# Performance work log

Measured on AMD Instinct MI355X. Metric: run time of the kernel, lower is better.

## Reference

```python
import jax, jax.numpy as jnp
import numpy as np

B, N = 8, 50000
NB, NA, NT, NI, NC = 60000, 120000, 180000, 20000, 1500000


def _term_index(key, n_terms, arity, n_atoms):
    # distinct atom indices per term (avoids degenerate zero-length vectors)
    k1, k2 = jax.random.split(key)
    base = jax.random.randint(k1, (n_terms,), 0, n_atoms)
    cols = [base]
    for a in range(arity - 1):
        off = jax.random.randint(jax.random.fold_in(k2, a), (n_terms,), 1, n_atoms)
        cols.append((base + off + a) % n_atoms)
    return jnp.stack(cols, axis=1).astype(jnp.int32)


def setup_inputs() -> dict:
    key = jax.random.key(0)
    ks = jax.random.split(key, 24)
    u = lambda k, s, lo, hi: jax.random.uniform(k, s, jnp.float32, lo, hi)
    coords = jax.random.normal(ks[0], (B, N, 3), jnp.float32) * 10.0
    return dict(
        coords=coords,
        bond_index=_term_index(ks[1], NB, 2, N),
        bond_rest_length=u(ks[2], (NB,), 1.0, 2.0),
        bond_force_constant=u(ks[3], (NB,), 200.0, 800.0),
        angle_index=_term_index(ks[4], NA, 3, N),
        angle_force_constant=u(ks[5], (NA,), 50.0, 300.0),
        angle_c0=u(ks[6], (NA,), 0.5, 2.0),
        angle_c1=u(ks[7], (NA,), -1.0, 1.0),
        angle_c2=u(ks[8], (NA,), -1.0, 1.0),
        torsion_index=_term_index(ks[9], NT, 4, N),
        torsion_force_constant=u(ks[10], (NT,), 1.0, 20.0),
        torsion_order=jax.random.randint(ks[11], (NT,), 1, 7).astype(jnp.int32),
        torsion_cos_term=jnp.where(jax.random.bernoulli(ks[12], 0.5, (NT,)), 1.0, -1.0).astype(jnp.float32),
        inversion_index=_term_index(ks[13], NI, 4, N),
        inversion_force_constant=u(ks[14], (NI,), 1.0, 40.0),
        inversion_c0=u(ks[15], (NI,), 0.5, 1.5),
        inversion_c1=u(ks[16], (NI,), -1.0, 1.0),
        inversion_c2=u(ks[17], (NI,), -1.0, 1.0),
        nonbond_index=_term_index(ks[18], NC, 2, N),
        vdw_minimum=u(ks[19], (NC,), 3.0, 4.0),
        vdw_well_depth=u(ks[20], (NC,), 0.01, 0.2),
        vdw_threshold_sq=jnp.square(u(ks[21], (NC,), 10.0, 30.0)),
    )


def _uff_energy(coords, bond_index, bond_rest_length, bond_force_constant,
                angle_index, angle_force_constant, angle_c0, angle_c1, angle_c2,
                torsion_index, torsion_force_constant, torsion_order, torsion_cos_term,
                inversion_index, inversion_force_constant, inversion_c0, inversion_c1, inversion_c2,
                nonbond_index, vdw_minimum, vdw_well_depth, vdw_threshold_sq):
    take = lambda idx: jnp.take(coords, idx, axis=1)  # (B, P, 3)

    # ---- bond stretch: 0.5 * k * (|r_ij| - r0)^2 ----
    d = take(bond_index[:, 0]) - take(bond_index[:, 1])
    dist = jnp.sqrt(jnp.sum(d * d, -1))
    e_bond = jnp.sum(0.5 * bond_force_constant * jnp.square(dist - bond_rest_length), -1)

    # ---- angle bend (general cosine expansion, order == 0 branch) ----
    p1, p2, p3 = take(angle_index[:, 0]), take(angle_index[:, 1]), take(angle_index[:, 2])
    v1, v2 = p1 - p2, p3 - p2
    dot = jnp.sum(v1 * v2, -1)
    inv = jax.lax.rsqrt(jnp.maximum(jnp.sum(v1 * v1, -1) * jnp.sum(v2 * v2, -1), 1e-24))
    ct = jnp.clip(dot * inv, -0.999999, 0.999999)
    cs = ct * ct
    ss = jnp.maximum(1.0 - cs, 1e-12)
    e_angle = jnp.sum(angle_force_constant * (angle_c0 + angle_c1 * ct + angle_c2 * (cs - ss)), -1)

    # ---- torsion: 0.5 * V * (1 - cos_term * cos(n * phi)) ----
    q1, q2, q3, q4 = (take(torsion_index[:, a]) for a in range(4))
    b1, b2, b3 = q2 - q1, q3 - q2, q4 - q3
    n1 = jnp.cross(b1, b2)
    n2 = jnp.cross(b2, b3)
    cn = jnp.sum(n1 * n2, -1) * jax.lax.rsqrt(
        jnp.maximum(jnp.sum(n1 * n1, -1) * jnp.sum(n2 * n2, -1), 1e-24))
    phi = jnp.arccos(jnp.clip(cn, -0.999999, 0.999999))
    n_f = torsion_order.astype(coords.dtype)
    e_tor = jnp.sum(0.5 * torsion_force_constant * (1.0 - torsion_cos_term * jnp.cos(n_f * phi)), -1)

    # ---- inversion (Wilson angle): K*(c0 + c1*sinY + c2*(2*sinY^2 - 1)), central atom = col 1 ----
    cA = take(inversion_index[:, 1])
    rji = take(inversion_index[:, 0]) - cA
    rjk = take(inversion_index[:, 2]) - cA
    rjl = take(inversion_index[:, 3]) - cA
    nrm = jnp.cross(rji, rjk)
    cosY = jnp.sum(nrm * rjl, -1) * jax.lax.rsqrt(
        jnp.maximum(jnp.sum(nrm * nrm, -1) * jnp.sum(rjl * rjl, -1), 1e-24))
    cosY = jnp.clip(cosY, -0.999999, 0.999999)
    sinY = jnp.sqrt(jnp.maximum(1.0 - cosY * cosY, 0.0))
    e_inv = jnp.sum(inversion_force_constant * (inversion_c0 + inversion_c1 * sinY
                                                + inversion_c2 * (2.0 * sinY * sinY - 1.0)), -1)

    # ---- vdW LJ on radius-graph candidates: D*((R/r)^12 - 2*(R/r)^6) within cutoff ----
    dnb = take(nonbond_index[:, 0]) - take(nonbond_index[:, 1])
    d2 = jnp.sum(dnb * dnb, -1)
    within = d2 <= vdw_threshold_sq  # pair selection done under no_grad in the original
    x2 = jnp.square(vdw_minimum) / jnp.maximum(d2, 1e-12)
    x6 = x2 * x2 * x2
    e_pair = vdw_well_depth * (x6 * x6 - 2.0 * x6)
    e_vdw = jnp.sum(jnp.where(within, e_pair, 0.0), -1)

    return e_bond + e_angle + e_tor + e_inv + e_vdw  # (B,)


def reference(coords, bond_index, bond_rest_length, bond_force_constant,
              angle_index, angle_force_constant, angle_c0, angle_c1, angle_c2,
              torsion_index, torsion_force_constant, torsion_order, torsion_cos_term,
              inversion_index, inversion_force_constant, inversion_c0, inversion_c1, inversion_c2,
              nonbond_index, vdw_minimum, vdw_well_depth, vdw_threshold_sq):
    return _uff_energy(coords, bond_index, bond_rest_length, bond_force_constant,
                       angle_index, angle_force_constant, angle_c0, angle_c1, angle_c2,
                       torsion_index, torsion_force_constant, torsion_order, torsion_cos_term,
                       inversion_index, inversion_force_constant, inversion_c0, inversion_c1, inversion_c2,
                       nonbond_index, vdw_minimum, vdw_well_depth, vdw_threshold_sq)
```

## Files before the change

kernel.cpp:

```cpp
#include <hip/hip_runtime.h>

#define TPB 256
#define NWAVE (TPB / 64)
#define CHUNK 256
#define GRID_MAIN 2048

typedef int vi2 __attribute__((ext_vector_type(2)));
typedef int vi4 __attribute__((ext_vector_type(4)));

struct SegInfo {
    int cb, ca, ct, ci, cl;
    int NB, NA, NT, NI, NC;
    int N;
};

__device__ __forceinline__ float clamp1(float x) {
    return fminf(fmaxf(x, -0.999999f), 0.999999f);
}

__device__ __forceinline__ float ntf(const float* p) { return __builtin_nontemporal_load(p); }

template <bool USE_WS>
__device__ __forceinline__ float4 loadC(const float4* __restrict__ cw,
                                        const float* __restrict__ coords,
                                        int N, int atom, int b) {
    if (USE_WS) {
        return cw[((size_t)atom << 3) + b];
    } else {
        const float* sp = coords + ((size_t)b * N + atom) * 3;
        return make_float4(sp[0], sp[1], sp[2], 0.f);
    }
}

__global__ void __launch_bounds__(TPB) transpose_coords(const float* __restrict__ coords,
                                                        float4* __restrict__ cw,
                                                        float* __restrict__ out, int N) {
    const int a = blockIdx.x * TPB + threadIdx.x;
    if (blockIdx.x == 0 && threadIdx.x < 8) out[threadIdx.x] = 0.f;
    if (a >= N) return;
#pragma unroll
    for (int b = 0; b < 8; b++) {
        const float* sp = coords + ((size_t)b * N + a) * 3;
        cw[((size_t)a << 3) + b] = make_float4(ntf(sp), ntf(sp + 1), ntf(sp + 2), 0.f);
    }
}

template <bool USE_WS>
__global__ void __launch_bounds__(TPB) uff_kernel(
    const float* __restrict__ coords, const float4* __restrict__ cw,
    const int* __restrict__ bidx, const float* __restrict__ br0, const float* __restrict__ bk,
    const int* __restrict__ aidx, const float* __restrict__ ak,
    const float* __restrict__ ac0, const float* __restrict__ ac1, const float* __restrict__ ac2,
    const int* __restrict__ tidx, const float* __restrict__ tk,
    const int* __restrict__ tord, const float* __restrict__ tcos,
    const int* __restrict__ iidx, const float* __restrict__ ik,
    const float* __restrict__ ic0, const float* __restrict__ ic1, const float* __restrict__ ic2,
    const int* __restrict__ nidx, const float* __restrict__ vmin,
    const float* __restrict__ vdep, const float* __restrict__ vthr,
    float* __restrict__ out, SegInfo s)
{
    __shared__ int4   sI[CHUNK];
    __shared__ float4 sP[CHUNK];

    const int tid = threadIdx.x;
    const int lane = tid & 63;
    const int b = tid & 7;
    const int g = tid >> 3;
    const int N = s.N;
    float acc = 0.f;

    for (int c = blockIdx.x; c < s.cb; c += gridDim.x) {
        const int base = c * CHUNK;
        {
            const int u = min(base + tid, s.NB - 1);
            const vi2 ij = __builtin_nontemporal_load((const vi2*)bidx + u);
            sI[tid] = make_int4(ij.x, ij.y, 0, 0);
            sP[tid] = make_float4(ntf(br0 + u), ntf(bk + u), 0.f, 0.f);
        }
        __syncthreads();
#pragma unroll 2
        for (int j = 0; j < 8; j++) {
            const int slot = g + 32 * j;
            const int4 q = sI[slot];
            const float4 p = sP[slot];
            float4 ci = loadC<USE_WS>(cw, coords, N, q.x, b);
            float4 cj = loadC<USE_WS>(cw, coords, N, q.y, b);
            float dx = ci.x - cj.x, dy = ci.y - cj.y, dz = ci.z - cj.z;
            float dd = sqrtf(dx * dx + dy * dy + dz * dz) - p.x;
            if (base + slot < s.NB) acc += 0.5f * p.y * dd * dd;
        }
        __syncthreads();
    }

    for (int c = blockIdx.x; c < s.ca; c += gridDim.x) {
        const int base = c * CHUNK;
        {
            const int u = min(base + tid, s.NA - 1);
            sI[tid] = make_int4(aidx[3 * u], aidx[3 * u + 1], aidx[3 * u + 2], 0);
            sP[tid] = make_float4(ntf(ak + u), ntf(ac0 + u), ntf(ac1 + u), ntf(ac2 + u));
        }
        __syncthreads();
#pragma unroll 2
        for (int j = 0; j < 8; j++) {
            const int slot = g + 32 * j;
            const int4 q = sI[slot];
            const float4 p = sP[slot];
            float4 P = loadC<USE_WS>(cw, coords, N, q.x, b);
            float4 Q = loadC<USE_WS>(cw, coords, N, q.y, b);
            float4 R = loadC<USE_WS>(cw, coords, N, q.z, b);
            float ax = P.x - Q.x, ay = P.y - Q.y, az = P.z - Q.z;
            float bx = R.x - Q.x, by = R.y - Q.y, bz = R.z - Q.z;
            float dot = ax * bx + ay * by + az * bz;
            float nn = (ax * ax + ay * ay + az * az) * (bx * bx + by * by + bz * bz);
            float ct = clamp1(dot * rsqrtf(fmaxf(nn, 1e-24f)));
            float cs = ct * ct;
            float sb = fmaxf(1.f - cs, 1e-12f);
            if (base + slot < s.NA) acc += p.x * (p.y + p.z * ct + p.w * (cs - sb));
        }
        __syncthreads();
    }

    for (int c = blockIdx.x; c < s.ct; c += gridDim.x) {
        const int base = c * CHUNK;
        {
            const int u = min(base + tid, s.NT - 1);
            const vi4 q = __builtin_nontemporal_load((const vi4*)tidx + u);
            sI[tid] = make_int4(q.x, q.y, q.z, q.w);
            sP[tid] = make_float4(ntf(tk + u), ntf(tcos + u),
                                  __int_as_float(__builtin_nontemporal_load(tord + u)), 0.f);
        }
        __syncthreads();
#pragma unroll 2
        for (int j = 0; j < 8; j++) {
            const int slot = g + 32 * j;
            const int4 q = sI[slot];
            const float4 p = sP[slot];
            const int ord = __float_as_int(p.z);
            float4 P1 = loadC<USE_WS>(cw, coords, N, q.x, b);
            float4 P2 = loadC<USE_WS>(cw, coords, N, q.y, b);
            float4 P3 = loadC<USE_WS>(cw, coords, N, q.z, b);
            float4 P4 = loadC<USE_WS>(cw, coords, N, q.w, b);
            float b1x = P2.x - P1.x, b1y = P2.y - P1.y, b1z = P2.z - P1.z;
            float b2x = P3.x - P2.x, b2y = P3.y - P2.y, b2z = P3.z - P2.z;
            float b3x = P4.x - P3.x, b3y = P4.y - P3.y, b3z = P4.z - P3.z;
            float n1x = b1y * b2z - b1z * b2y;
            float n1y = b1z * b2x - b1x * b2z;
            float n1z = b1x * b2y - b1y * b2x;
            float n2x = b2y * b3z - b2z * b3y;
            float n2y = b2z * b3x - b2x * b3z;
            float n2z = b2x * b3y - b2y * b3x;
            float dot = n1x * n2x + n1y * n2y + n1z * n2z;
            float nn = (n1x * n1x + n1y * n1y + n1z * n1z) *
                       (n2x * n2x + n2y * n2y + n2z * n2z);
            float x = clamp1(dot * rsqrtf(fmaxf(nn, 1e-24f)));
            float Tp = 1.f, Tc = x, res = x;
#pragma unroll
            for (int kk = 2; kk <= 6; kk++) {
                float Tn = 2.f * x * Tc - Tp;
                Tp = Tc; Tc = Tn;
                if (ord == kk) res = Tn;
            }
            if (base + slot < s.NT) acc += 0.5f * p.x * (1.f - p.y * res);
        }
        __syncthreads();
    }

    for (int c = blockIdx.x; c < s.ci; c += gridDim.x) {
        const int base = c * CHUNK;
        {
            const int u = min(base + tid, s.NI - 1);
            const vi4 q = __builtin_nontemporal_load((const vi4*)iidx + u);
            sI[tid] = make_int4(q.x, q.y, q.z, q.w);
            sP[tid] = make_float4(ntf(ik + u), ntf(ic0 + u), ntf(ic1 + u), ntf(ic2 + u));
        }
        __syncthreads();
#pragma unroll 2
        for (int j = 0; j < 8; j++) {
            const int slot = g + 32 * j;
            const int4 q = sI[slot];
            const float4 p = sP[slot];
            float4 CA = loadC<USE_WS>(cw, coords, N, q.y, b);
            float4 PI = loadC<USE_WS>(cw, coords, N, q.x, b);
            float4 PK = loadC<USE_WS>(cw, coords, N, q.z, b);
            float4 PL = loadC<USE_WS>(cw, coords, N, q.w, b);
            float jix = PI.x - CA.x, jiy = PI.y - CA.y, jiz = PI.z - CA.z;
            float jkx = PK.x - CA.x, jky = PK.y - CA.y, jkz = PK.z - CA.z;
            float lx  = PL.x - CA.x, ly  = PL.y - CA.y, lz  = PL.z - CA.z;
            float nx = jiy * jkz - jiz * jky;
            float ny = jiz * jkx - jix * jkz;
            float nz = jix * jky - jiy * jkx;
            float dot = nx * lx + ny * ly + nz * lz;
            float nn = (nx * nx + ny * ny + nz * nz) * (lx * lx + ly * ly + lz * lz);
            float cosY = clamp1(dot * rsqrtf(fmaxf(nn, 1e-24f)));
            float sinY = sqrtf(fmaxf(1.f - cosY * cosY, 0.f));
            if (base + slot < s.NI) acc += p.x * (p.y + p.z * sinY + p.w * (2.f * sinY * sinY - 1.f));
        }
        __syncthreads();
    }

    for (int c = blockIdx.x; c < s.cl; c += gridDim.x) {
        const int base = c * CHUNK;
        {
            const int u = min(base + tid, s.NC - 1);
            const vi2 ij = __builtin_nontemporal_load((const vi2*)nidx + u);
            const float R = ntf(vmin + u);
            sI[tid] = make_int4(ij.x, ij.y, 0, 0);
            sP[tid] = make_float4(R * R, ntf(vdep + u), ntf(vthr + u), 0.f);
        }
        __syncthreads();
#pragma unroll
        for (int j = 0; j < 8; j += 2) {
            const int s0 = g + 32 * j, s1 = s0 + 32;
            const int4 q0 = sI[s0]; const float4 p0 = sP[s0];
            const int4 q1 = sI[s1]; const float4 p1 = sP[s1];
            float4 a0 = loadC<USE_WS>(cw, coords, N, q0.x, b);
            float4 b0 = loadC<USE_WS>(cw, coords, N, q0.y, b);
            float4 a1 = loadC<USE_WS>(cw, coords, N, q1.x, b);
            float4 b1 = loadC<USE_WS>(cw, coords, N, q1.y, b);
            {
                float dx = a0.x - b0.x, dy = a0.y - b0.y, dz = a0.z - b0.z;
                float d2 = dx * dx + dy * dy + dz * dz;
                float x2 = p0.x / fmaxf(d2, 1e-12f);
                float x6 = x2 * x2 * x2;
                float e = p0.y * (x6 * x6 - 2.f * x6);
                if (base + s0 < s.NC && d2 <= p0.z) acc += e;
            }
            {
                float dx = a1.x - b1.x, dy = a1.y - b1.y, dz = a1.z - b1.z;
                float d2 = dx * dx + dy * dy + dz * dz;
                float x2 = p1.x / fmaxf(d2, 1e-12f);
                float x6 = x2 * x2 * x2;
                float e = p1.y * (x6 * x6 - 2.f * x6);
                if (base + s1 < s.NC && d2 <= p1.z) acc += e;
            }
        }
        __syncthreads();
    }

    float v = acc;
    v += __shfl_down(v, 8, 64);
    v += __shfl_down(v, 16, 64);
    v += __shfl_down(v, 32, 64);

    __shared__ float red[NWAVE][8];
    const int wid = tid >> 6;
    if (lane < 8) red[wid][lane] = v;
    __syncthreads();
    if (tid < 8) {
        float ssum = 0.f;
#pragma unroll
        for (int w = 0; w < NWAVE; w++) ssum += red[w][tid];
        atomicAdd(&out[tid], ssum);
    }
}

static inline int cdiv(int a, int b) { return (a + b - 1) / b; }

extern "C" void kernel_launch(void* const* d_in, const int* in_sizes, int n_in,
                              void* d_out, int out_size, void* d_ws, size_t ws_size,
                              hipStream_t stream) {
    const int B = out_size;
    const int NB = in_sizes[2], NA = in_sizes[5], NT = in_sizes[10],
              NI = in_sizes[14], NC = in_sizes[19];
    const int N = in_sizes[0] / (3 * B);

    const float* coords = (const float*)d_in[0];
    const int*   bidx = (const int*)d_in[1];
    const float* br0  = (const float*)d_in[2];
    const float* bk   = (const float*)d_in[3];
    const int*   aidx = (const int*)d_in[4];
    const float* ak   = (const float*)d_in[5];
    const float* ac0  = (const float*)d_in[6];
    const float* ac1  = (const float*)d_in[7];
    const float* ac2  = (const float*)d_in[8];
    const int*   tidx = (const int*)d_in[9];
    const float* tk   = (const float*)d_in[10];
    const int*   tord = (const int*)d_in[11];
    const float* tcos = (const float*)d_in[12];
    const int*   iidx = (const int*)d_in[13];
    const float* ik   = (const float*)d_in[14];
    const float* ic0  = (const float*)d_in[15];
    const float* ic1  = (const float*)d_in[16];
    const float* ic2  = (const float*)d_in[17];
    const int*   nidx = (const int*)d_in[18];
    const float* vmin = (const float*)d_in[19];
    const float* vdep = (const float*)d_in[20];
    const float* vthr = (const float*)d_in[21];

    const size_t ws_need = (size_t)N * 8 * sizeof(float4);
    const bool use_ws = ws_size >= ws_need;
    float4* cw = (float4*)d_ws;

    if (use_ws) {
        transpose_coords<<<cdiv(N, TPB), TPB, 0, stream>>>(coords, cw, (float*)d_out, N);
    } else {
        hipMemsetAsync(d_out, 0, (size_t)out_size * sizeof(float), stream);
    }

    SegInfo s;
    s.NB = NB; s.NA = NA; s.NT = NT; s.NI = NI; s.NC = NC; s.N = N;
    s.cb = cdiv(NB, CHUNK);
    s.ca = cdiv(NA, CHUNK);
    s.ct = cdiv(NT, CHUNK);
    s.ci = cdiv(NI, CHUNK);
    s.cl = cdiv(NC, CHUNK);

    if (use_ws) {
        uff_kernel<true><<<GRID_MAIN, TPB, 0, stream>>>(
            coords, cw, bidx, br0, bk, aidx, ak, ac0, ac1, ac2,
            tidx, tk, tord, tcos, iidx, ik, ic0, ic1, ic2,
            nidx, vmin, vdep, vthr, (float*)d_out, s);
    } else {
        uff_kernel<false><<<GRID_MAIN, TPB, 0, stream>>>(
            coords, cw, bidx, br0, bk, aidx, ak, ac0, ac1, ac2,
            tidx, tk, tord, tcos, iidx, ik, ic0, ic1, ic2,
            nidx, vmin, vdep, vthr, (float*)d_out, s);
    }
}
```

Before: 168.8 us.

## Replace block-strided chunk loops with per-wave dynamic work stealing via atomic counter

Each wavefront now grabs 64-term chunks from a global atomic counter across a unified index space covering all five term types. This replaces the static block-strided loops and their block-wide __syncthreads with per-wave shared staging. The aim is to remove load imbalance between blocks and the barrier stalls between segments. The cost is one atomic per 64 terms, which is about 37k atomics on a single counter, plus branching over the term kind per chunk.

```diff
diff --git a/kernel.cpp b/kernel.cpp
--- a/kernel.cpp
+++ b/kernel.cpp
@@ -2,7 +2,6 @@
 
 #define TPB 256
 #define NWAVE (TPB / 64)
-#define CHUNK 256
 #define GRID_MAIN 2048
 
 typedef int vi2 __attribute__((ext_vector_type(2)));
@@ -19,6 +18,7 @@
 }
 
 __device__ __forceinline__ float ntf(const float* p) { return __builtin_nontemporal_load(p); }
+__device__ __forceinline__ int   nti(const int* p)   { return __builtin_nontemporal_load(p); }
 
 template <bool USE_WS>
 __device__ __forceinline__ float4 loadC(const float4* __restrict__ cw,
@@ -34,9 +34,13 @@
 
 __global__ void __launch_bounds__(TPB) transpose_coords(const float* __restrict__ coords,
                                                         float4* __restrict__ cw,
-                                                        float* __restrict__ out, int N) {
+                                                        float* __restrict__ out,
+                                                        int* __restrict__ ctr, int N) {
     const int a = blockIdx.x * TPB + threadIdx.x;
-    if (blockIdx.x == 0 && threadIdx.x < 8) out[threadIdx.x] = 0.f;
+    if (blockIdx.x == 0) {
+        if (threadIdx.x < 8) out[threadIdx.x] = 0.f;
+        if (threadIdx.x == 8) *ctr = 0;
+    }
     if (a >= N) return;
 #pragma unroll
     for (int b = 0; b < 8; b++) {
@@ -57,184 +61,173 @@
     const float* __restrict__ ic0, const float* __restrict__ ic1, const float* __restrict__ ic2,
     const int* __restrict__ nidx, const float* __restrict__ vmin,
     const float* __restrict__ vdep, const float* __restrict__ vthr,
-    float* __restrict__ out, SegInfo s)
+    int* __restrict__ ctr, float* __restrict__ out, SegInfo s)
 {
-    __shared__ int4   sI[CHUNK];
-    __shared__ float4 sP[CHUNK];
+    __shared__ int4   sI[NWAVE][64];
+    __shared__ float4 sP[NWAVE][64];
 
     const int tid = threadIdx.x;
     const int lane = tid & 63;
-    const int b = tid & 7;
-    const int g = tid >> 3;
+    const int w = tid >> 6;
+    const int b = lane & 7;
+    const int gw = lane >> 3;
     const int N = s.N;
     float acc = 0.f;
 
-    for (int c = blockIdx.x; c < s.cb; c += gridDim.x) {
-        const int base = c * CHUNK;
-        {
-            const int u = min(base + tid, s.NB - 1);
+    int4*   mI = sI[w];
+    float4* mP = sP[w];
+
+    while (true) {
+        int c = 0;
+        if (lane == 0) c = atomicAdd(ctr, 1);
+        c = __shfl(c, 0, 64);
+        if (c >= s.cl) break;
+
+        int kind, base;
+        if (c < s.cb)      { kind = 0; base = c * 64; }
+        else if (c < s.ca) { kind = 1; base = (c - s.cb) * 64; }
+        else if (c < s.ct) { kind = 2; base = (c - s.ca) * 64; }
+        else if (c < s.ci) { kind = 3; base = (c - s.ct) * 64; }
+        else               { kind = 4; base = (c - s.ci) * 64; }
+
+        if (kind == 0) {
+            const int u = min(base + lane, s.NB - 1);
             const vi2 ij = __builtin_nontemporal_load((const vi2*)bidx + u);
-            sI[tid] = make_int4(ij.x, ij.y, 0, 0);
-            sP[tid] = make_float4(ntf(br0 + u), ntf(bk + u), 0.f, 0.f);
-        }
-        __syncthreads();
-#pragma unroll 2
-        for (int j = 0; j < 8; j++) {
-            const int slot = g + 32 * j;
-            const int4 q = sI[slot];
-            const float4 p = sP[slot];
-            float4 ci = loadC<USE_WS>(cw, coords, N, q.x, b);
-            float4 cj = loadC<USE_WS>(cw, coords, N, q.y, b);
-            float dx = ci.x - cj.x, dy = ci.y - cj.y, dz = ci.z - cj.z;
-            float dd = sqrtf(dx * dx + dy * dy + dz * dz) - p.x;
-            if (base + slot < s.NB) acc += 0.5f * p.y * dd * dd;
-        }
-        __syncthreads();
-    }
-
-    for (int c = blockIdx.x; c < s.ca; c += gridDim.x) {
-        const int base = c * CHUNK;
-        {
-            const int u = min(base + tid, s.NA - 1);
-            sI[tid] = make_int4(aidx[3 * u], aidx[3 * u + 1], aidx[3 * u + 2], 0);
-            sP[tid] = make_float4(ntf(ak + u), ntf(ac0 + u), ntf(ac1 + u), ntf(ac2 + u));
-        }
-        __syncthreads();
-#pragma unroll 2
-        for (int j = 0; j < 8; j++) {
-            const int slot = g + 32 * j;
-            const int4 q = sI[slot];
-            const float4 p = sP[slot];
-            float4 P = loadC<USE_WS>(cw, coords, N, q.x, b);
-            float4 Q = loadC<USE_WS>(cw, coords, N, q.y, b);
-            float4 R = loadC<USE_WS>(cw, coords, N, q.z, b);
-            float ax = P.x - Q.x, ay = P.y - Q.y, az = P.z - Q.z;
-            float bx = R.x - Q.x, by = R.y - Q.y, bz = R.z - Q.z;
-            float dot = ax * bx + ay * by + az * bz;
-            float nn = (ax * ax + ay * ay + az * az) * (bx * bx + by * by + bz * bz);
-            float ct = clamp1(dot * rsqrtf(fmaxf(nn, 1e-24f)));
-            float cs = ct * ct;
-            float sb = fmaxf(1.f - cs, 1e-12f);
-            if (base + slot < s.NA) acc += p.x * (p.y + p.z * ct + p.w * (cs - sb));
-        }
-        __syncthreads();
-    }
-
-    for (int c = blockIdx.x; c < s.ct; c += gridDim.x) {
-        const int base = c * CHUNK;
-        {
-            const int u = min(base + tid, s.NT - 1);
+            mI[lane] = make_int4(ij.x, ij.y, 0, 0);
+            mP[lane] = make_float4(ntf(br0 + u), ntf(bk + u), 0.f, 0.f);
+        } else if (kind == 1) {
+            const int u = min(base + lane, s.NA - 1);
+            mI[lane] = make_int4(aidx[3 * u], aidx[3 * u + 1], aidx[3 * u + 2], 0);
+            mP[lane] = make_float4(ntf(ak + u), ntf(ac0 + u), ntf(ac1 + u), ntf(ac2 + u));
+        } else if (kind == 2) {
+            const int u = min(base + lane, s.NT - 1);
             const vi4 q = __builtin_nontemporal_load((const vi4*)tidx + u);
-            sI[tid] = make_int4(q.x, q.y, q.z, q.w);
-            sP[tid] = make_float4(ntf(tk + u), ntf(tcos + u),
-                                  __int_as_float(__builtin_nontemporal_load(tord + u)), 0.f);
-        }
-        __syncthreads();
-#pragma unroll 2
-        for (int j = 0; j < 8; j++) {
-            const int slot = g + 32 * j;
-            const int4 q = sI[slot];
-            const float4 p = sP[slot];
-            const int ord = __float_as_int(p.z);
-            float4 P1 = loadC<USE_WS>(cw, coords, N, q.x, b);
-            float4 P2 = loadC<USE_WS>(cw, coords, N, q.y, b);
-            float4 P3 = loadC<USE_WS>(cw, coords, N, q.z, b);
-            float4 P4 = loadC<USE_WS>(cw, coords, N, q.w, b);
-            float b1x = P2.x - P1.x, b1y = P2.y - P1.y, b1z = P2.z - P1.z;
-            float b2x = P3.x - P2.x, b2y = P3.y - P2.y, b2z = P3.z - P2.z;
-            float b3x = P4.x - P3.x, b3y = P4.y - P3.y, b3z = P4.z - P3.z;
-            float n1x = b1y * b2z - b1z * b2y;
-            float n1y = b1z * b2x - b1x * b2z;
-            float n1z = b1x * b2y - b1y * b2x;
-            float n2x = b2y * b3z - b2z * b3y;
-            float n2y = b2z * b3x - b2x * b3z;
-            float n2z = b2x * b3y - b2y * b3x;
-            float dot = n1x * n2x + n1y * n2y + n1z * n2z;
-            float nn = (n1x * n1x + n1y * n1y + n1z * n1z) *
-                       (n2x * n2x + n2y * n2y + n2z * n2z);
-            float x = clamp1(dot * rsqrtf(fmaxf(nn, 1e-24f)));
-            float Tp = 1.f, Tc = x, res = x;
-#pragma unroll
-            for (int kk = 2; kk <= 6; kk++) {
-                float Tn = 2.f * x * Tc - Tp;
-                Tp = Tc; Tc = Tn;
-                if (ord == kk) res = Tn;
-            }
-            if (base + slot < s.NT) acc += 0.5f * p.x * (1.f - p.y * res);
-        }
-        __syncthreads();
-    }
-
-    for (int c = blockIdx.x; c < s.ci; c += gridDim.x) {
-        const int base = c * CHUNK;
-        {
-            const int u = min(base + tid, s.NI - 1);
+            mI[lane] = make_int4(q.x, q.y, q.z, q.w);
+            mP[lane] = make_float4(ntf(tk + u), ntf(tcos + u),
+                                   __int_as_float(nti(tord + u)), 0.f);
+        } else if (kind == 3) {
+            const int u = min(base + lane, s.NI - 1);
             const vi4 q = __builtin_nontemporal_load((const vi4*)iidx + u);
-            sI[tid] = make_int4(q.x, q.y, q.z, q.w);
-            sP[tid] = make_float4(ntf(ik + u), ntf(ic0 + u), ntf(ic1 + u), ntf(ic2 + u));
-        }
-        __syncthreads();
-#pragma unroll 2
-        for (int j = 0; j < 8; j++) {
-            const int slot = g + 32 * j;
-            const int4 q = sI[slot];
-            const float4 p = sP[slot];
-            float4 CA = loadC<USE_WS>(cw, coords, N, q.y, b);
-            float4 PI = loadC<USE_WS>(cw, coords, N, q.x, b);
-            float4 PK = loadC<USE_WS>(cw, coords, N, q.z, b);
-            float4 PL = loadC<USE_WS>(cw, coords, N, q.w, b);
-            float jix = PI.x - CA.x, jiy = PI.y - CA.y, jiz = PI.z - CA.z;
-            float jkx = PK.x - CA.x, jky = PK.y - CA.y, jkz = PK.z - CA.z;
-            float lx  = PL.x - CA.x, ly  = PL.y - CA.y, lz  = PL.z - CA.z;
-            float nx = jiy * jkz - jiz * jky;
-            float ny = jiz * jkx - jix * jkz;
-            float nz = jix * jky - jiy * jkx;
-            float dot = nx * lx + ny * ly + nz * lz;
-            float nn = (nx * nx + ny * ny + nz * nz) * (lx * lx + ly * ly + lz * lz);
-            float cosY = clamp1(dot * rsqrtf(fmaxf(nn, 1e-24f)));
-            float sinY = sqrtf(fmaxf(1.f - cosY * cosY, 0.f));
-            if (base + slot < s.NI) acc += p.x * (p.y + p.z * sinY + p.w * (2.f * sinY * sinY - 1.f));
-        }
-        __syncthreads();
-    }
-
-    for (int c = blockIdx.x; c < s.cl; c += gridDim.x) {
-        const int base = c * CHUNK;
-        {
-            const int u = min(base + tid, s.NC - 1);
+            mI[lane] = make_int4(q.x, q.y, q.z, q.w);
+            mP[lane] = make_float4(ntf(ik + u), ntf(ic0 + u), ntf(ic1 + u), ntf(ic2 + u));
+        } else {
+            const int u = min(base + lane, s.NC - 1);
             const vi2 ij = __builtin_nontemporal_load((const vi2*)nidx + u);
             const float R = ntf(vmin + u);
-            sI[tid] = make_int4(ij.x, ij.y, 0, 0);
-            sP[tid] = make_float4(R * R, ntf(vdep + u), ntf(vthr + u), 0.f);
+            mI[lane] = make_int4(ij.x, ij.y, 0, 0);
+            mP[lane] = make_float4(R * R, ntf(vdep + u), ntf(vthr + u), 0.f);
         }
-        __syncthreads();
+
+        if (kind == 4) {
 #pragma unroll
-        for (int j = 0; j < 8; j += 2) {
-            const int s0 = g + 32 * j, s1 = s0 + 32;
-            const int4 q0 = sI[s0]; const float4 p0 = sP[s0];
-            const int4 q1 = sI[s1]; const float4 p1 = sP[s1];
-            float4 a0 = loadC<USE_WS>(cw, coords, N, q0.x, b);
-            float4 b0 = loadC<USE_WS>(cw, coords, N, q0.y, b);
-            float4 a1 = loadC<USE_WS>(cw, coords, N, q1.x, b);
-            float4 b1 = loadC<USE_WS>(cw, coords, N, q1.y, b);
-            {
-                float dx = a0.x - b0.x, dy = a0.y - b0.y, dz = a0.z - b0.z;
-                float d2 = dx * dx + dy * dy + dz * dz;
-                float x2 = p0.x / fmaxf(d2, 1e-12f);
-                float x6 = x2 * x2 * x2;
-                float e = p0.y * (x6 * x6 - 2.f * x6);
-                if (base + s0 < s.NC && d2 <= p0.z) acc += e;
-            }
-            {
-                float dx = a1.x - b1.x, dy = a1.y - b1.y, dz = a1.z - b1.z;
-                float d2 = dx * dx + dy * dy + dz * dz;
-                float x2 = p1.x / fmaxf(d2, 1e-12f);
-                float x6 = x2 * x2 * x2;
-                float e = p1.y * (x6 * x6 - 2.f * x6);
-                if (base + s1 < s.NC && d2 <= p1.z) acc += e;
+            for (int j = 0; j < 4; j++) {
+                const int s0 = j * 8 + gw, s1 = s0 + 32;
+                const int4 q0 = mI[s0]; const float4 p0 = mP[s0];
+                const int4 q1 = mI[s1]; const float4 p1 = mP[s1];
+                float4 a0 = loadC<USE_WS>(cw, coords, N, q0.x, b);
+                float4 b0 = loadC<USE_WS>(cw, coords, N, q0.y, b);
+                float4 a1 = loadC<USE_WS>(cw, coords, N, q1.x, b);
+                float4 b1 = loadC<USE_WS>(cw, coords, N, q1.y, b);
+                {
+                    float dx = a0.x - b0.x, dy = a0.y - b0.y, dz = a0.z - b0.z;
+                    float d2 = dx * dx + dy * dy + dz * dz;
+                    float x2 = p0.x / fmaxf(d2, 1e-12f);
+                    float x6 = x2 * x2 * x2;
+                    float e = p0.y * (x6 * x6 - 2.f * x6);
+                    if (base + s0 < s.NC && d2 <= p0.z) acc += e;
+                }
+                {
+                    float dx = a1.x - b1.x, dy = a1.y - b1.y, dz = a1.z - b1.z;
+                    float d2 = dx * dx + dy * dy + dz * dz;
+                    float x2 = p1.x / fmaxf(d2, 1e-12f);
+                    float x6 = x2 * x2 * x2;
+                    float e = p1.y * (x6 * x6 - 2.f * x6);
+                    if (base + s1 < s.NC && d2 <= p1.z) acc += e;
+                }
+            }
+        } else if (kind == 0) {
+#pragma unroll 2
+            for (int j = 0; j < 8; j++) {
+                const int slot = j * 8 + gw;
+                const int4 q = mI[slot]; const float4 p = mP[slot];
+                float4 ci = loadC<USE_WS>(cw, coords, N, q.x, b);
+                float4 cj = loadC<USE_WS>(cw, coords, N, q.y, b);
+                float dx = ci.x - cj.x, dy = ci.y - cj.y, dz = ci.z - cj.z;
+                float dd = sqrtf(dx * dx + dy * dy + dz * dz) - p.x;
+                if (base + slot < s.NB) acc += 0.5f * p.y * dd * dd;
+            }
+        } else if (kind == 1) {
+#pragma unroll 2
+            for (int j = 0; j < 8; j++) {
+                const int slot = j * 8 + gw;
+                const int4 q = mI[slot]; const float4 p = mP[slot];
+                float4 P = loadC<USE_WS>(cw, coords, N, q.x, b);
+                float4 Q = loadC<USE_WS>(cw, coords, N, q.y, b);
+                float4 R = loadC<USE_WS>(cw, coords, N, q.z, b);
+                float ax = P.x - Q.x, ay = P.y - Q.y, az = P.z - Q.z;
+                float bx = R.x - Q.x, by = R.y - Q.y, bz = R.z - Q.z;
+                float dot = ax * bx + ay * by + az * bz;
+                float nn = (ax * ax + ay * ay + az * az) * (bx * bx + by * by + bz * bz);
+                float ct = clamp1(dot * rsqrtf(fmaxf(nn, 1e-24f)));
+                float cs = ct * ct;
+                float sb = fmaxf(1.f - cs, 1e-12f);
+                if (base + slot < s.NA) acc += p.x * (p.y + p.z * ct + p.w * (cs - sb));
+            }
+        } else if (kind == 2) {
+#pragma unroll 2
+            for (int j = 0; j < 8; j++) {
+                const int slot = j * 8 + gw;
+                const int4 q = mI[slot]; const float4 p = mP[slot];
+                const int ord = __float_as_int(p.z);
+                float4 P1 = loadC<USE_WS>(cw, coords, N, q.x, b);
+                float4 P2 = loadC<USE_WS>(cw, coords, N, q.y, b);
+                float4 P3 = loadC<USE_WS>(cw, coords, N, q.z, b);
+                float4 P4 = loadC<USE_WS>(cw, coords, N, q.w, b);
+                float b1x = P2.x - P1.x, b1y = P2.y - P1.y, b1z = P2.z - P1.z;
+                float b2x = P3.x - P2.x, b2y = P3.y - P2.y, b2z = P3.z - P2.z;
+                float b3x = P4.x - P3.x, b3y = P4.y - P3.y, b3z = P4.z - P3.z;
+                float n1x = b1y * b2z - b1z * b2y;
+                float n1y = b1z * b2x - b1x * b2z;
+                float n1z = b1x * b2y - b1y * b2x;
+                float n2x = b2y * b3z - b2z * b3y;
+                float n2y = b2z * b3x - b2x * b3z;
+                float n2z = b2x * b3y - b2y * b3x;
+                float dot = n1x * n2x + n1y * n2y + n1z * n2z;
+                float nn = (n1x * n1x + n1y * n1y + n1z * n1z) *
+                           (n2x * n2x + n2y * n2y + n2z * n2z);
+                float x = clamp1(dot * rsqrtf(fmaxf(nn, 1e-24f)));
+                float Tp = 1.f, Tc = x, res = x;
+#pragma unroll
+                for (int kk = 2; kk <= 6; kk++) {
+                    float Tn = 2.f * x * Tc - Tp;
+                    Tp = Tc; Tc = Tn;
+                    if (ord == kk) res = Tn;
+                }
+                if (base + slot < s.NT) acc += 0.5f * p.x * (1.f - p.y * res);
+            }
+        } else {
+#pragma unroll 2
+            for (int j = 0; j < 8; j++) {
+                const int slot = j * 8 + gw;
+                const int4 q = mI[slot]; const float4 p = mP[slot];
+                float4 CA = loadC<USE_WS>(cw, coords, N, q.y, b);
+                float4 PI = loadC<USE_WS>(cw, coords, N, q.x, b);
+                float4 PK = loadC<USE_WS>(cw, coords, N, q.z, b);
+                float4 PL = loadC<USE_WS>(cw, coords, N, q.w, b);
+                float jix = PI.x - CA.x, jiy = PI.y - CA.y, jiz = PI.z - CA.z;
+                float jkx = PK.x - CA.x, jky = PK.y - CA.y, jkz = PK.z - CA.z;
+                float lx  = PL.x - CA.x, ly  = PL.y - CA.y, lz  = PL.z - CA.z;
+                float nx = jiy * jkz - jiz * jky;
+                float ny = jiz * jkx - jix * jkz;
+                float nz = jix * jky - jiy * jkx;
+                float dot = nx * lx + ny * ly + nz * lz;
+                float nn = (nx * nx + ny * ny + nz * nz) * (lx * lx + ly * ly + lz * lz);
+                float cosY = clamp1(dot * rsqrtf(fmaxf(nn, 1e-24f)));
+                float sinY = sqrtf(fmaxf(1.f - cosY * cosY, 0.f));
+                if (base + slot < s.NI)
+                    acc += p.x * (p.y + p.z * sinY + p.w * (2.f * sinY * sinY - 1.f));
             }
         }
-        __syncthreads();
     }
 
     float v = acc;
@@ -243,13 +236,12 @@
     v += __shfl_down(v, 32, 64);
 
     __shared__ float red[NWAVE][8];
-    const int wid = tid >> 6;
-    if (lane < 8) red[wid][lane] = v;
+    if (lane < 8) red[w][lane] = v;
     __syncthreads();
     if (tid < 8) {
         float ssum = 0.f;
 #pragma unroll
-        for (int w = 0; w < NWAVE; w++) ssum += red[w][tid];
+        for (int i = 0; i < NWAVE; i++) ssum += red[i][tid];
         atomicAdd(&out[tid], ssum);
     }
 }
@@ -287,33 +279,37 @@
     const float* vdep = (const float*)d_in[20];
     const float* vthr = (const float*)d_in[21];
 
-    const size_t ws_need = (size_t)N * 8 * sizeof(float4);
-    const bool use_ws = ws_size >= ws_need;
+    const size_t cw_bytes = (size_t)N * 8 * sizeof(float4);
+    const bool use_ws = ws_size >= cw_bytes + sizeof(int);
     float4* cw = (float4*)d_ws;
+    int* ctr;
 
     if (use_ws) {
-        transpose_coords<<<cdiv(N, TPB), TPB, 0, stream>>>(coords, cw, (float*)d_out, N);
+        ctr = (int*)((char*)d_ws + cw_bytes);
+        transpose_coords<<<cdiv(N, TPB), TPB, 0, stream>>>(coords, cw, (float*)d_out, ctr, N);
     } else {
+        ctr = (int*)d_ws;
         hipMemsetAsync(d_out, 0, (size_t)out_size * sizeof(float), stream);
+        hipMemsetAsync(d_ws, 0, sizeof(int), stream);
     }
 
     SegInfo s;
     s.NB = NB; s.NA = NA; s.NT = NT; s.NI = NI; s.NC = NC; s.N = N;
-    s.cb = cdiv(NB, CHUNK);
-    s.ca = cdiv(NA, CHUNK);
-    s.ct = cdiv(NT, CHUNK);
-    s.ci = cdiv(NI, CHUNK);
-    s.cl = cdiv(NC, CHUNK);
+    s.cb = cdiv(NB, 64);
+    s.ca = s.cb + cdiv(NA, 64);
+    s.ct = s.ca + cdiv(NT, 64);
+    s.ci = s.ct + cdiv(NI, 64);
+    s.cl = s.ci + cdiv(NC, 64);
 
     if (use_ws) {
         uff_kernel<true><<<GRID_MAIN, TPB, 0, stream>>>(
             coords, cw, bidx, br0, bk, aidx, ak, ac0, ac1, ac2,
             tidx, tk, tord, tcos, iidx, ik, ic0, ic1, ic2,
-            nidx, vmin, vdep, vthr, (float*)d_out, s);
+            nidx, vmin, vdep, vthr, ctr, (float*)d_out, s);
     } else {
         uff_kernel<false><<<GRID_MAIN, TPB, 0, stream>>>(
             coords, cw, bidx, br0, bk, aidx, ak, ac0, ac1, ac2,
             tidx, tk, tord, tcos, iidx, ik, ic0, ic1, ic2,
-            nidx, vmin, vdep, vthr, (float*)d_out, s);
-    }
-}
+            nidx, vmin, vdep, vthr, ctr, (float*)d_out, s);
+    }
+}
```

Result: slower. 555.3 us (+229.0%).
